# Kernel tuning notes

Measured on AMD Instinct MI355X. Metric: run time of the kernel, lower is better.

The kernel has to match this reference:

```python
import jax, jax.numpy as jnp
import numpy as np

LOG2PI = float(np.log(2.0 * np.pi))
B, D = 8192, 4096


def setup_inputs() -> dict:
    key = jax.random.key(0)
    k1, k2, k3, k4, k5 = jax.random.split(key, 5)
    return {
        "z": jax.random.normal(k1, (B, D), dtype=jnp.float32),
        "mean": jax.random.normal(k2, (B, D), dtype=jnp.float32),
        "log_sd": jax.random.normal(k3, (B, D), dtype=jnp.float32),
        "target": jax.random.randint(k4, (B,), 0, 2, dtype=jnp.int64 if jax.config.jax_enable_x64 else jnp.int32),
        "logdet": jax.random.normal(k5, (B,), dtype=jnp.float32),
    }


def reference(z, mean, log_sd, target, logdet):
    # Per-class (binary) masked statistics, exactly matching the torch forward:
    #   mu_cls = mean[target==j].mean(0); log_sd_cls likewise;
    #   log_p  = gaussian_log_p(z_cls, mu_cls, log_sd_cls).sum(feature).mean(batch)
    def per_class(j):
        m = (target == j).astype(z.dtype)          # (B,)
        cnt = m.sum()
        ld_mean = (logdet * m).sum() / cnt          # scalar
        mu = (mean * m[:, None]).sum(0) / cnt       # (D,)
        lsd = (log_sd * m[:, None]).sum(0) / cnt    # (D,)
        # gaussian log-prob summed over features, per sample -> (B,)
        lp = (-0.5 * LOG2PI - lsd
              - 0.5 * (z - mu) ** 2 * jnp.exp(-2.0 * lsd)).sum(1)
        lp_mean = (lp * m).sum() / cnt              # masked mean over class members
        return ld_mean, mu, lsd, lp_mean

    res = [per_class(j) for j in (0, 1)]
    logdet_total = jnp.stack([r[0] for r in res])   # (2,)
    mus_per_class = jnp.stack([r[1] for r in res])  # (2, D)
    log_sds_per_class = jnp.stack([r[2] for r in res])  # (2, D)
    log_p_total = jnp.stack([r[3] for r in res])    # (2,)
    prior_logprob = (log_p_total + logdet_total).mean()
    return prior_logprob, mus_per_class, log_sds_per_class, log_p_total
```

## Files before the change

### kernel.cpp

```cpp
#include <hip/hip_runtime.h>

#define B_SZ 8192
#define D_SZ 4096
#define PC   128
#define RP   (B_SZ / PC)

typedef float f32x4 __attribute__((ext_vector_type(4)));
typedef int   i32x4 __attribute__((ext_vector_type(4)));


__global__ __launch_bounds__(256, 4)
void stage1_kernel(const float* __restrict__ z,
                   const float* __restrict__ mean,
                   const float* __restrict__ lsd,
                   const int* __restrict__ target,
                   const float* __restrict__ logdet,
                   float* __restrict__ part,
                   float* __restrict__ sc) {
    if (blockIdx.x == 4 * PC) {
        __shared__ float rsm[3][4];
        float c = 0.f, a = 0.f, o = 0.f;
#pragma unroll
        for (int k = 0; k < 8; ++k) {
            const int i = k * 1024 + (threadIdx.x << 2);
            const i32x4 t = *(const i32x4*)(target + i);
            const f32x4 l = *(const f32x4*)(logdet + i);
            const float n0 = (t.x == 1) ? 1.f : 0.f;
            const float n1 = (t.y == 1) ? 1.f : 0.f;
            const float n2 = (t.z == 1) ? 1.f : 0.f;
            const float n3 = (t.w == 1) ? 1.f : 0.f;
            c += n0 + n1 + n2 + n3;
            a += l.x + l.y + l.z + l.w;
            o += l.x * n0 + l.y * n1 + l.z * n2 + l.w * n3;
        }
        for (int off = 32; off > 0; off >>= 1) {
            c += __shfl_down(c, off);
            a += __shfl_down(a, off);
            o += __shfl_down(o, off);
        }
        const int w = threadIdx.x >> 6;
        if ((threadIdx.x & 63) == 0) { rsm[0][w] = c; rsm[1][w] = a; rsm[2][w] = o; }
        __syncthreads();
        if (threadIdx.x == 0) {
            sc[0] = rsm[0][0] + rsm[0][1] + rsm[0][2] + rsm[0][3];
            sc[1] = rsm[1][0] + rsm[1][1] + rsm[1][2] + rsm[1][3];
            sc[2] = rsm[2][0] + rsm[2][1] + rsm[2][2] + rsm[2][3];
        }
        return;
    }

    const int col = (blockIdx.x & 3) * 1024 + (threadIdx.x << 2);
    const int r   = blockIdx.x >> 2;
    const size_t base0 = (size_t)(r * RP) * D_SZ + col;

    const float* pz = z    + base0;
    const float* pm = mean + base0;
    const float* pl = lsd  + base0;
    const int*   pt = target + r * RP;

    f32x4 mA = 0, m1 = 0, lA = 0, l1 = 0;
    f32x4 zA = 0, z1 = 0, qA = 0, q1 = 0;

#pragma unroll 1
    for (int it = 0; it < RP / 4; ++it) {
        f32x4 vz0 = *(const f32x4*)(pz);
        f32x4 vz1 = *(const f32x4*)(pz + 1 * D_SZ);
        f32x4 vz2 = *(const f32x4*)(pz + 2 * D_SZ);
        f32x4 vz3 = *(const f32x4*)(pz + 3 * D_SZ);
        f32x4 vm0 = *(const f32x4*)(pm);
        f32x4 vm1 = *(const f32x4*)(pm + 1 * D_SZ);
        f32x4 vm2 = *(const f32x4*)(pm + 2 * D_SZ);
        f32x4 vm3 = *(const f32x4*)(pm + 3 * D_SZ);
        f32x4 vl0 = *(const f32x4*)(pl);
        f32x4 vl1 = *(const f32x4*)(pl + 1 * D_SZ);
        f32x4 vl2 = *(const f32x4*)(pl + 2 * D_SZ);
        f32x4 vl3 = *(const f32x4*)(pl + 3 * D_SZ);
        i32x4 t   = *(const i32x4*)(pt);
        asm volatile("" : "+v"(vz0), "+v"(vz1), "+v"(vz2), "+v"(vz3),
                          "+v"(vm0), "+v"(vm1), "+v"(vm2), "+v"(vm3),
                          "+v"(vl0), "+v"(vl1), "+v"(vl2), "+v"(vl3),
                          "+v"(t));

        const float k0 = (t.x == 1) ? 1.f : 0.f;
        const float k1 = (t.y == 1) ? 1.f : 0.f;
        const float k2 = (t.z == 1) ? 1.f : 0.f;
        const float k3 = (t.w == 1) ? 1.f : 0.f;

        mA += vm0; m1 += vm0 * k0;
        mA += vm1; m1 += vm1 * k1;
        mA += vm2; m1 += vm2 * k2;
        mA += vm3; m1 += vm3 * k3;

        lA += vl0; l1 += vl0 * k0;
        lA += vl1; l1 += vl1 * k1;
        lA += vl2; l1 += vl2 * k2;
        lA += vl3; l1 += vl3 * k3;

        zA += vz0; z1 += vz0 * k0;
        zA += vz1; z1 += vz1 * k1;
        zA += vz2; z1 += vz2 * k2;
        zA += vz3; z1 += vz3 * k3;

        const f32x4 q0 = vz0 * vz0; qA += q0; q1 += q0 * k0;
        const f32x4 qb = vz1 * vz1; qA += qb; q1 += qb * k1;
        const f32x4 qc = vz2 * vz2; qA += qc; q1 += qc * k2;
        const f32x4 qd = vz3 * vz3; qA += qd; q1 += qd * k3;

        pz += 4 * D_SZ; pm += 4 * D_SZ; pl += 4 * D_SZ; pt += 4;
    }

    *(f32x4*)(part + ((size_t)(0 * PC + r)) * D_SZ + col) = mA;
    *(f32x4*)(part + ((size_t)(1 * PC + r)) * D_SZ + col) = m1;
    *(f32x4*)(part + ((size_t)(2 * PC + r)) * D_SZ + col) = lA;
    *(f32x4*)(part + ((size_t)(3 * PC + r)) * D_SZ + col) = l1;
    *(f32x4*)(part + ((size_t)(4 * PC + r)) * D_SZ + col) = zA;
    *(f32x4*)(part + ((size_t)(5 * PC + r)) * D_SZ + col) = z1;
    *(f32x4*)(part + ((size_t)(6 * PC + r)) * D_SZ + col) = qA;
    *(f32x4*)(part + ((size_t)(7 * PC + r)) * D_SZ + col) = q1;
}

__global__ __launch_bounds__(256)
void reduce_kernel(const float* __restrict__ part,
                   float* __restrict__ red) {
    const int seg  = blockIdx.x >> 3;
    const int rem  = blockIdx.x & 7;
    const int col  = (rem >> 1) * 1024 + (threadIdx.x << 2);
    const int half = rem & 1;
    f32x4 acc = 0;
    for (int r = half * (PC / 2); r < (half + 1) * (PC / 2); ++r) {
        acc += *(const f32x4*)(part + ((size_t)seg * PC + r) * D_SZ + col);
    }
    *(f32x4*)(red + ((size_t)(half * 8 + seg)) * D_SZ + col) = acc;
}

__global__ __launch_bounds__(256)
void finalize_cols_kernel(const float* __restrict__ red,
                          const float* __restrict__ sc,
                          double* __restrict__ dslots,
                          float* __restrict__ out) {
    const int d = blockIdx.x * 256 + threadIdx.x;
    const float cnt1 = sc[0];
    const float cnt0 = (float)B_SZ - cnt1;

#define RSEG(s) (red[(s) * D_SZ + d] + red[(8 + (s)) * D_SZ + d])
    const float ma = RSEG(0), m1 = RSEG(1);
    const float la = RSEG(2), l1 = RSEG(3);
    const float za = RSEG(4), z1 = RSEG(5);
    const float qa = RSEG(6), q1 = RSEG(7);
#undef RSEG

    const float mu1 = m1 / cnt1, mu0 = (ma - m1) / cnt0;
    const float ls1 = l1 / cnt1, ls0 = (la - l1) / cnt0;

    out[1 + d]            = mu0;
    out[1 + D_SZ + d]     = mu1;
    out[1 + 2 * D_SZ + d] = ls0;
    out[1 + 3 * D_SZ + d] = ls1;

    const float z0 = za - z1, q0 = qa - q1;
    const double w0 = 0.5 * exp(-2.0 * (double)ls0);
    const double w1 = 0.5 * exp(-2.0 * (double)ls1);
    double S0 = w0 * ((double)q0 - 2.0 * (double)mu0 * (double)z0 + (double)cnt0 * (double)mu0 * (double)mu0);
    double S1 = w1 * ((double)q1 - 2.0 * (double)mu1 * (double)z1 + (double)cnt1 * (double)mu1 * (double)mu1);
    double L0 = (double)ls0;
    double L1 = (double)ls1;

    for (int off = 32; off > 0; off >>= 1) {
        S0 += __shfl_down(S0, off);
        S1 += __shfl_down(S1, off);
        L0 += __shfl_down(L0, off);
        L1 += __shfl_down(L1, off);
    }
    if ((threadIdx.x & 63) == 0) {
        double* wd = dslots + (blockIdx.x * 4 + (threadIdx.x >> 6)) * 4;
        wd[0] = S0; wd[1] = S1; wd[2] = L0; wd[3] = L1;
    }
}

__global__ void finalize_scalars_kernel(const float* __restrict__ sc,
                                        const double* __restrict__ dslots,
                                        float* __restrict__ out) {
    const double* p = dslots + threadIdx.x * 4;
    double S0 = p[0], S1 = p[1], L0 = p[2], L1 = p[3];
    for (int off = 32; off > 0; off >>= 1) {
        S0 += __shfl_down(S0, off);
        S1 += __shfl_down(S1, off);
        L0 += __shfl_down(L0, off);
        L1 += __shfl_down(L1, off);
    }
    if (threadIdx.x == 0) {
        const double LOG2PI = 1.8378770664093453;
        const double cnt1 = (double)sc[0];
        const double cnt0 = (double)B_SZ - cnt1;
        const double ldm1 = (double)sc[2] / cnt1;
        const double ldm0 = ((double)sc[1] - (double)sc[2]) / cnt0;

        const double c0 = -0.5 * LOG2PI * (double)D_SZ - L0;
        const double c1 = -0.5 * LOG2PI * (double)D_SZ - L1;
        const double lp0 = c0 - S0 / cnt0;
        const double lp1 = c1 - S1 / cnt1;

        out[1 + 4 * D_SZ + 0] = (float)lp0;
        out[1 + 4 * D_SZ + 1] = (float)lp1;
        out[0] = (float)(0.5 * ((lp0 + ldm0) + (lp1 + ldm1)));
    }
}

extern "C" void kernel_launch(void* const* d_in, const int* in_sizes, int n_in,
                              void* d_out, int out_size, void* d_ws, size_t ws_size,
                              hipStream_t stream) {
    const float* z      = (const float*)d_in[0];
    const float* mean   = (const float*)d_in[1];
    const float* log_sd = (const float*)d_in[2];
    const int*   target = (const int*)d_in[3];
    const float* logdet = (const float*)d_in[4];
    float* out = (float*)d_out;
    float* ws  = (float*)d_ws;

    float*  part   = ws;
    float*  red    = ws + (size_t)PC * 8 * D_SZ;
    float*  sc     = red + 16 * D_SZ;
    double* dslots = (double*)(sc + 8);

    stage1_kernel<<<4 * PC + 1, 256, 0, stream>>>(z, mean, log_sd, target, logdet, part, sc);
    reduce_kernel<<<64, 256, 0, stream>>>(part, red);
    finalize_cols_kernel<<<D_SZ / 256, 256, 0, stream>>>(red, sc, dslots, out);
    finalize_scalars_kernel<<<1, 64, 0, stream>>>(sc, dslots, out);
}
```

Measured before the change: 87.27 us.

## Fuse four kernels into one persistent kernel with atomic-counter grid barriers

Merges the stage-1 accumulation, partial reduction, per-column finalize and scalar finalize into a single launch. Blocks signal completion through agent-scope atomic counters, and the lower-indexed blocks spin-wait before each later stage. This removes three kernel launches and their inter-kernel gaps, at the cost of a memset launch and spin-waiting. It relies on all 513 blocks being co-resident, which 256 CUs at 4 blocks per CU should allow, otherwise it could deadlock.

```diff
diff --git a/kernel.cpp b/kernel.cpp
--- a/kernel.cpp
+++ b/kernel.cpp
@@ -4,21 +4,45 @@
 #define D_SZ 4096
 #define PC   128
 #define RP   (B_SZ / PC)
+#define NCOLSUM (4 * PC)
+#define GRID_SZ (NCOLSUM + 1)
 
 typedef float f32x4 __attribute__((ext_vector_type(4)));
 typedef int   i32x4 __attribute__((ext_vector_type(4)));
 
 
+__device__ __forceinline__ void fence_arrive(int* ctr) {
+    __syncthreads();
+    if (threadIdx.x == 0) {
+        __threadfence();
+        __hip_atomic_fetch_add(ctr, 1, __ATOMIC_ACQ_REL, __HIP_MEMORY_SCOPE_AGENT);
+    }
+}
+__device__ __forceinline__ void spin_wait(int* ctr, int target) {
+    if (threadIdx.x == 0) {
+        while (__hip_atomic_load(ctr, __ATOMIC_ACQUIRE, __HIP_MEMORY_SCOPE_AGENT) < target) {
+            __builtin_amdgcn_s_sleep(2);
+        }
+    }
+    __syncthreads();
+}
+
 __global__ __launch_bounds__(256, 4)
-void stage1_kernel(const float* __restrict__ z,
-                   const float* __restrict__ mean,
-                   const float* __restrict__ lsd,
-                   const int* __restrict__ target,
-                   const float* __restrict__ logdet,
-                   float* __restrict__ part,
-                   float* __restrict__ sc) {
-    if (blockIdx.x == 4 * PC) {
-        __shared__ float rsm[3][4];
+void fused_kernel(const float* __restrict__ z,
+                  const float* __restrict__ mean,
+                  const float* __restrict__ lsd,
+                  const int* __restrict__ target,
+                  const float* __restrict__ logdet,
+                  float* __restrict__ part,
+                  float* __restrict__ red,
+                  float* __restrict__ sc,
+                  double* __restrict__ dslots,
+                  int* __restrict__ ctrs,
+                  float* __restrict__ out) {
+    const int bid = blockIdx.x;
+    __shared__ float rsm[3][4];
+
+    if (bid == NCOLSUM) {
         float c = 0.f, a = 0.f, o = 0.f;
 #pragma unroll
         for (int k = 0; k < 8; ++k) {
@@ -46,163 +70,167 @@
             sc[1] = rsm[1][0] + rsm[1][1] + rsm[1][2] + rsm[1][3];
             sc[2] = rsm[2][0] + rsm[2][1] + rsm[2][2] + rsm[2][3];
         }
+        fence_arrive(&ctrs[0]);
         return;
     }
 
-    const int col = (blockIdx.x & 3) * 1024 + (threadIdx.x << 2);
-    const int r   = blockIdx.x >> 2;
-    const size_t base0 = (size_t)(r * RP) * D_SZ + col;
-
-    const float* pz = z    + base0;
-    const float* pm = mean + base0;
-    const float* pl = lsd  + base0;
-    const int*   pt = target + r * RP;
-
-    f32x4 mA = 0, m1 = 0, lA = 0, l1 = 0;
-    f32x4 zA = 0, z1 = 0, qA = 0, q1 = 0;
+    {
+        const int col = (bid & 3) * 1024 + (threadIdx.x << 2);
+        const int r   = bid >> 2;
+        const size_t base0 = (size_t)(r * RP) * D_SZ + col;
+
+        const float* pz = z    + base0;
+        const float* pm = mean + base0;
+        const float* pl = lsd  + base0;
+        const int*   pt = target + r * RP;
+
+        f32x4 mA = 0, m1 = 0, lA = 0, l1 = 0;
+        f32x4 zA = 0, z1 = 0, qA = 0, q1 = 0;
 
 #pragma unroll 1
-    for (int it = 0; it < RP / 4; ++it) {
-        f32x4 vz0 = *(const f32x4*)(pz);
-        f32x4 vz1 = *(const f32x4*)(pz + 1 * D_SZ);
-        f32x4 vz2 = *(const f32x4*)(pz + 2 * D_SZ);
-        f32x4 vz3 = *(const f32x4*)(pz + 3 * D_SZ);
-        f32x4 vm0 = *(const f32x4*)(pm);
-        f32x4 vm1 = *(const f32x4*)(pm + 1 * D_SZ);
-        f32x4 vm2 = *(const f32x4*)(pm + 2 * D_SZ);
-        f32x4 vm3 = *(const f32x4*)(pm + 3 * D_SZ);
-        f32x4 vl0 = *(const f32x4*)(pl);
-        f32x4 vl1 = *(const f32x4*)(pl + 1 * D_SZ);
-        f32x4 vl2 = *(const f32x4*)(pl + 2 * D_SZ);
-        f32x4 vl3 = *(const f32x4*)(pl + 3 * D_SZ);
-        i32x4 t   = *(const i32x4*)(pt);
-        asm volatile("" : "+v"(vz0), "+v"(vz1), "+v"(vz2), "+v"(vz3),
-                          "+v"(vm0), "+v"(vm1), "+v"(vm2), "+v"(vm3),
-                          "+v"(vl0), "+v"(vl1), "+v"(vl2), "+v"(vl3),
-                          "+v"(t));
-
-        const float k0 = (t.x == 1) ? 1.f : 0.f;
-        const float k1 = (t.y == 1) ? 1.f : 0.f;
-        const float k2 = (t.z == 1) ? 1.f : 0.f;
-        const float k3 = (t.w == 1) ? 1.f : 0.f;
-
-        mA += vm0; m1 += vm0 * k0;
-        mA += vm1; m1 += vm1 * k1;
-        mA += vm2; m1 += vm2 * k2;
-        mA += vm3; m1 += vm3 * k3;
-
-        lA += vl0; l1 += vl0 * k0;
-        lA += vl1; l1 += vl1 * k1;
-        lA += vl2; l1 += vl2 * k2;
-        lA += vl3; l1 += vl3 * k3;
-
-        zA += vz0; z1 += vz0 * k0;
-        zA += vz1; z1 += vz1 * k1;
-        zA += vz2; z1 += vz2 * k2;
-        zA += vz3; z1 += vz3 * k3;
-
-        const f32x4 q0 = vz0 * vz0; qA += q0; q1 += q0 * k0;
-        const f32x4 qb = vz1 * vz1; qA += qb; q1 += qb * k1;
-        const f32x4 qc = vz2 * vz2; qA += qc; q1 += qc * k2;
-        const f32x4 qd = vz3 * vz3; qA += qd; q1 += qd * k3;
-
-        pz += 4 * D_SZ; pm += 4 * D_SZ; pl += 4 * D_SZ; pt += 4;
-    }
-
-    *(f32x4*)(part + ((size_t)(0 * PC + r)) * D_SZ + col) = mA;
-    *(f32x4*)(part + ((size_t)(1 * PC + r)) * D_SZ + col) = m1;
-    *(f32x4*)(part + ((size_t)(2 * PC + r)) * D_SZ + col) = lA;
-    *(f32x4*)(part + ((size_t)(3 * PC + r)) * D_SZ + col) = l1;
-    *(f32x4*)(part + ((size_t)(4 * PC + r)) * D_SZ + col) = zA;
-    *(f32x4*)(part + ((size_t)(5 * PC + r)) * D_SZ + col) = z1;
-    *(f32x4*)(part + ((size_t)(6 * PC + r)) * D_SZ + col) = qA;
-    *(f32x4*)(part + ((size_t)(7 * PC + r)) * D_SZ + col) = q1;
-}
-
-__global__ __launch_bounds__(256)
-void reduce_kernel(const float* __restrict__ part,
-                   float* __restrict__ red) {
-    const int seg  = blockIdx.x >> 3;
-    const int rem  = blockIdx.x & 7;
-    const int col  = (rem >> 1) * 1024 + (threadIdx.x << 2);
-    const int half = rem & 1;
-    f32x4 acc = 0;
-    for (int r = half * (PC / 2); r < (half + 1) * (PC / 2); ++r) {
-        acc += *(const f32x4*)(part + ((size_t)seg * PC + r) * D_SZ + col);
-    }
-    *(f32x4*)(red + ((size_t)(half * 8 + seg)) * D_SZ + col) = acc;
-}
-
-__global__ __launch_bounds__(256)
-void finalize_cols_kernel(const float* __restrict__ red,
-                          const float* __restrict__ sc,
-                          double* __restrict__ dslots,
-                          float* __restrict__ out) {
-    const int d = blockIdx.x * 256 + threadIdx.x;
-    const float cnt1 = sc[0];
-    const float cnt0 = (float)B_SZ - cnt1;
+        for (int it = 0; it < RP / 4; ++it) {
+            f32x4 vz0 = *(const f32x4*)(pz);
+            f32x4 vz1 = *(const f32x4*)(pz + 1 * D_SZ);
+            f32x4 vz2 = *(const f32x4*)(pz + 2 * D_SZ);
+            f32x4 vz3 = *(const f32x4*)(pz + 3 * D_SZ);
+            f32x4 vm0 = *(const f32x4*)(pm);
+            f32x4 vm1 = *(const f32x4*)(pm + 1 * D_SZ);
+            f32x4 vm2 = *(const f32x4*)(pm + 2 * D_SZ);
+            f32x4 vm3 = *(const f32x4*)(pm + 3 * D_SZ);
+            f32x4 vl0 = *(const f32x4*)(pl);
+            f32x4 vl1 = *(const f32x4*)(pl + 1 * D_SZ);
+            f32x4 vl2 = *(const f32x4*)(pl + 2 * D_SZ);
+            f32x4 vl3 = *(const f32x4*)(pl + 3 * D_SZ);
+            i32x4 t   = *(const i32x4*)(pt);
+            asm volatile("" : "+v"(vz0), "+v"(vz1), "+v"(vz2), "+v"(vz3),
+                              "+v"(vm0), "+v"(vm1), "+v"(vm2), "+v"(vm3),
+                              "+v"(vl0), "+v"(vl1), "+v"(vl2), "+v"(vl3),
+                              "+v"(t));
+
+            const float k0 = (t.x == 1) ? 1.f : 0.f;
+            const float k1 = (t.y == 1) ? 1.f : 0.f;
+            const float k2 = (t.z == 1) ? 1.f : 0.f;
+            const float k3 = (t.w == 1) ? 1.f : 0.f;
+
+            mA += vm0; m1 += vm0 * k0;
+            mA += vm1; m1 += vm1 * k1;
+            mA += vm2; m1 += vm2 * k2;
+            mA += vm3; m1 += vm3 * k3;
+
+            lA += vl0; l1 += vl0 * k0;
+            lA += vl1; l1 += vl1 * k1;
+            lA += vl2; l1 += vl2 * k2;
+            lA += vl3; l1 += vl3 * k3;
+
+            zA += vz0; z1 += vz0 * k0;
+            zA += vz1; z1 += vz1 * k1;
+            zA += vz2; z1 += vz2 * k2;
+            zA += vz3; z1 += vz3 * k3;
+
+            const f32x4 q0 = vz0 * vz0; qA += q0; q1 += q0 * k0;
+            const f32x4 qb = vz1 * vz1; qA += qb; q1 += qb * k1;
+            const f32x4 qc = vz2 * vz2; qA += qc; q1 += qc * k2;
+            const f32x4 qd = vz3 * vz3; qA += qd; q1 += qd * k3;
+
+            pz += 4 * D_SZ; pm += 4 * D_SZ; pl += 4 * D_SZ; pt += 4;
+        }
+
+        *(f32x4*)(part + ((size_t)(0 * PC + r)) * D_SZ + col) = mA;
+        *(f32x4*)(part + ((size_t)(1 * PC + r)) * D_SZ + col) = m1;
+        *(f32x4*)(part + ((size_t)(2 * PC + r)) * D_SZ + col) = lA;
+        *(f32x4*)(part + ((size_t)(3 * PC + r)) * D_SZ + col) = l1;
+        *(f32x4*)(part + ((size_t)(4 * PC + r)) * D_SZ + col) = zA;
+        *(f32x4*)(part + ((size_t)(5 * PC + r)) * D_SZ + col) = z1;
+        *(f32x4*)(part + ((size_t)(6 * PC + r)) * D_SZ + col) = qA;
+        *(f32x4*)(part + ((size_t)(7 * PC + r)) * D_SZ + col) = q1;
+    }
+    fence_arrive(&ctrs[0]);
+    if (bid >= 64) return;
+
+    spin_wait(&ctrs[0], GRID_SZ);
+    {
+        const int seg  = bid >> 3;
+        const int rem  = bid & 7;
+        const int col  = (rem >> 1) * 1024 + (threadIdx.x << 2);
+        const int half = rem & 1;
+        f32x4 acc = 0;
+        for (int r = half * (PC / 2); r < (half + 1) * (PC / 2); ++r) {
+            acc += *(const f32x4*)(part + ((size_t)seg * PC + r) * D_SZ + col);
+        }
+        *(f32x4*)(red + ((size_t)(half * 8 + seg)) * D_SZ + col) = acc;
+    }
+    fence_arrive(&ctrs[1]);
+    if (bid >= 16) return;
+
+    spin_wait(&ctrs[1], 64);
+    {
+        const int d = bid * 256 + threadIdx.x;
+        const float cnt1 = sc[0];
+        const float cnt0 = (float)B_SZ - cnt1;
 
 #define RSEG(s) (red[(s) * D_SZ + d] + red[(8 + (s)) * D_SZ + d])
-    const float ma = RSEG(0), m1 = RSEG(1);
-    const float la = RSEG(2), l1 = RSEG(3);
-    const float za = RSEG(4), z1 = RSEG(5);
-    const float qa = RSEG(6), q1 = RSEG(7);
+        const float ma = RSEG(0), m1 = RSEG(1);
+        const float la = RSEG(2), l1 = RSEG(3);
+        const float za = RSEG(4), z1 = RSEG(5);
+        const float qa = RSEG(6), q1 = RSEG(7);
 #undef RSEG
 
-    const float mu1 = m1 / cnt1, mu0 = (ma - m1) / cnt0;
-    const float ls1 = l1 / cnt1, ls0 = (la - l1) / cnt0;
-
-    out[1 + d]            = mu0;
-    out[1 + D_SZ + d]     = mu1;
-    out[1 + 2 * D_SZ + d] = ls0;
-    out[1 + 3 * D_SZ + d] = ls1;
-
-    const float z0 = za - z1, q0 = qa - q1;
-    const double w0 = 0.5 * exp(-2.0 * (double)ls0);
-    const double w1 = 0.5 * exp(-2.0 * (double)ls1);
-    double S0 = w0 * ((double)q0 - 2.0 * (double)mu0 * (double)z0 + (double)cnt0 * (double)mu0 * (double)mu0);
-    double S1 = w1 * ((double)q1 - 2.0 * (double)mu1 * (double)z1 + (double)cnt1 * (double)mu1 * (double)mu1);
-    double L0 = (double)ls0;
-    double L1 = (double)ls1;
-
-    for (int off = 32; off > 0; off >>= 1) {
-        S0 += __shfl_down(S0, off);
-        S1 += __shfl_down(S1, off);
-        L0 += __shfl_down(L0, off);
-        L1 += __shfl_down(L1, off);
-    }
-    if ((threadIdx.x & 63) == 0) {
-        double* wd = dslots + (blockIdx.x * 4 + (threadIdx.x >> 6)) * 4;
-        wd[0] = S0; wd[1] = S1; wd[2] = L0; wd[3] = L1;
-    }
-}
-
-__global__ void finalize_scalars_kernel(const float* __restrict__ sc,
-                                        const double* __restrict__ dslots,
-                                        float* __restrict__ out) {
-    const double* p = dslots + threadIdx.x * 4;
-    double S0 = p[0], S1 = p[1], L0 = p[2], L1 = p[3];
-    for (int off = 32; off > 0; off >>= 1) {
-        S0 += __shfl_down(S0, off);
-        S1 += __shfl_down(S1, off);
-        L0 += __shfl_down(L0, off);
-        L1 += __shfl_down(L1, off);
-    }
-    if (threadIdx.x == 0) {
-        const double LOG2PI = 1.8378770664093453;
-        const double cnt1 = (double)sc[0];
-        const double cnt0 = (double)B_SZ - cnt1;
-        const double ldm1 = (double)sc[2] / cnt1;
-        const double ldm0 = ((double)sc[1] - (double)sc[2]) / cnt0;
-
-        const double c0 = -0.5 * LOG2PI * (double)D_SZ - L0;
-        const double c1 = -0.5 * LOG2PI * (double)D_SZ - L1;
-        const double lp0 = c0 - S0 / cnt0;
-        const double lp1 = c1 - S1 / cnt1;
-
-        out[1 + 4 * D_SZ + 0] = (float)lp0;
-        out[1 + 4 * D_SZ + 1] = (float)lp1;
-        out[0] = (float)(0.5 * ((lp0 + ldm0) + (lp1 + ldm1)));
+        const float mu1 = m1 / cnt1, mu0 = (ma - m1) / cnt0;
+        const float ls1 = l1 / cnt1, ls0 = (la - l1) / cnt0;
+
+        out[1 + d]            = mu0;
+        out[1 + D_SZ + d]     = mu1;
+        out[1 + 2 * D_SZ + d] = ls0;
+        out[1 + 3 * D_SZ + d] = ls1;
+
+        const float z0 = za - z1, q0 = qa - q1;
+        const double w0 = 0.5 * exp(-2.0 * (double)ls0);
+        const double w1 = 0.5 * exp(-2.0 * (double)ls1);
+        double S0 = w0 * ((double)q0 - 2.0 * (double)mu0 * (double)z0 + (double)cnt0 * (double)mu0 * (double)mu0);
+        double S1 = w1 * ((double)q1 - 2.0 * (double)mu1 * (double)z1 + (double)cnt1 * (double)mu1 * (double)mu1);
+        double L0 = (double)ls0;
+        double L1 = (double)ls1;
+
+        for (int off = 32; off > 0; off >>= 1) {
+            S0 += __shfl_down(S0, off);
+            S1 += __shfl_down(S1, off);
+            L0 += __shfl_down(L0, off);
+            L1 += __shfl_down(L1, off);
+        }
+        if ((threadIdx.x & 63) == 0) {
+            double* wd = dslots + (bid * 4 + (threadIdx.x >> 6)) * 4;
+            wd[0] = S0; wd[1] = S1; wd[2] = L0; wd[3] = L1;
+        }
+    }
+    fence_arrive(&ctrs[2]);
+    if (bid >= 1) return;
+
+    spin_wait(&ctrs[2], 16);
+    if (threadIdx.x < 64) {
+        const double* p = dslots + threadIdx.x * 4;
+        double S0 = p[0], S1 = p[1], L0 = p[2], L1 = p[3];
+        for (int off = 32; off > 0; off >>= 1) {
+            S0 += __shfl_down(S0, off);
+            S1 += __shfl_down(S1, off);
+            L0 += __shfl_down(L0, off);
+            L1 += __shfl_down(L1, off);
+        }
+        if (threadIdx.x == 0) {
+            const double LOG2PI = 1.8378770664093453;
+            const double cnt1 = (double)sc[0];
+            const double cnt0 = (double)B_SZ - cnt1;
+            const double ldm1 = (double)sc[2] / cnt1;
+            const double ldm0 = ((double)sc[1] - (double)sc[2]) / cnt0;
+
+            const double c0 = -0.5 * LOG2PI * (double)D_SZ - L0;
+            const double c1 = -0.5 * LOG2PI * (double)D_SZ - L1;
+            const double lp0 = c0 - S0 / cnt0;
+            const double lp1 = c1 - S1 / cnt1;
+
+            out[1 + 4 * D_SZ + 0] = (float)lp0;
+            out[1 + 4 * D_SZ + 1] = (float)lp1;
+            out[0] = (float)(0.5 * ((lp0 + ldm0) + (lp1 + ldm1)));
+        }
     }
 }
 
@@ -221,9 +249,9 @@
     float*  red    = ws + (size_t)PC * 8 * D_SZ;
     float*  sc     = red + 16 * D_SZ;
     double* dslots = (double*)(sc + 8);
-
-    stage1_kernel<<<4 * PC + 1, 256, 0, stream>>>(z, mean, log_sd, target, logdet, part, sc);
-    reduce_kernel<<<64, 256, 0, stream>>>(part, red);
-    finalize_cols_kernel<<<D_SZ / 256, 256, 0, stream>>>(red, sc, dslots, out);
-    finalize_scalars_kernel<<<1, 64, 0, stream>>>(sc, dslots, out);
-}
+    int*    ctrs   = (int*)(dslots + 256);
+
+    hipMemsetAsync(ctrs, 0, 4 * sizeof(int), stream);
+    fused_kernel<<<GRID_SZ, 256, 0, stream>>>(z, mean, log_sd, target, logdet,
+                                              part, red, sc, dslots, ctrs, out);
+}
```

Result: slower. 149.2 us (+71.0%).
